# Performance work log

Measured on AMD Instinct MI355X. Metric: run time of the kernel, lower is better.

Reference implementation:

```python
import jax, jax.numpy as jnp
import numpy as np

B, IN, O = 256, 512, 10
STRUCTURES = list(range(32, 257, 32))  # 8 neuron structures
REPS, N_ACT = 4, 4


def _build_hidden_ids():
    ids = []
    i = 0
    # activation-major, then repetition, then structure (matches build_model_ids)
    for _ in range(N_ACT * REPS):
        for s in STRUCTURES:
            ids += [i] * s
            i += 1
    return np.asarray(ids, dtype=np.int32), i


def setup_inputs() -> dict:
    ids, M = _build_hidden_ids()
    H = len(ids)  # 18432
    k = jax.random.split(jax.random.key(0), 5)
    x = jax.random.normal(k[0], (B, IN), dtype=jnp.float32)
    hidden_w = jax.random.normal(k[1], (H, IN), dtype=jnp.float32) / np.sqrt(IN)
    hidden_b = jax.random.normal(k[2], (H,), dtype=jnp.float32) * 0.02
    out_w = jax.random.normal(k[3], (O, H), dtype=jnp.float32) * 0.05
    out_b = jax.random.normal(k[4], (M, O), dtype=jnp.float32) * 0.02
    return {"x": x, "hidden_w": hidden_w, "hidden_b": hidden_b,
            "out_w": out_w, "out_b": out_b,
            "hidden_ids": jnp.asarray(ids)}


_ACTS = [jax.nn.relu, jnp.tanh, jax.nn.sigmoid, lambda t: t]


def reference(x, hidden_w, hidden_b, out_w, out_b, hidden_ids):
    # hidden layer: [B, H]
    h = x @ hidden_w.T + hidden_b
    # per-activation contiguous splits (equal size H // n_act)
    chunks = jnp.split(h, N_ACT, axis=1)
    a = jnp.concatenate([f(c) for f, c in zip(_ACTS, chunks)], axis=1)  # [B, H]
    # per-hidden-neuron contribution to each output unit: [B, H, O]
    contrib = a[:, :, None] * out_w.T[None, :, :]
    M = out_b.shape[0]
    # segment-reduce hidden neurons into their model id: [M, B, O] -> [B, M, O]
    agg = jax.ops.segment_sum(contrib.transpose(1, 0, 2), hidden_ids, num_segments=M)
    return agg.transpose(1, 0, 2) + out_b[None, :, :]
```

## Files before the change

kernel.cpp:

```cpp
#include <hip/hip_runtime.h>
#include <hip/hip_bf16.h>

typedef __bf16 bf16x8 __attribute__((ext_vector_type(8)));
typedef float floatx4 __attribute__((ext_vector_type(4)));

#define BATCH 256
#define INDIM 512
#define ODIM 10
#define HTOT 18432
#define NMODEL 128
#define HTILE 64
#define BTILE 64
#define BK 64
#define LSTRIDE 72
#define ACT_CHUNK 4608
#define NJPG (HTOT / 32)

__device__ __forceinline__ unsigned pk2(float a, float b) {
    unsigned ua = __float_as_uint(a);
    ua = (ua + 0x7fffu + ((ua >> 16) & 1u)) >> 16;
    unsigned ub = __float_as_uint(b);
    ub = (ub + 0x7fffu + ((ub >> 16) & 1u)) >> 16;
    return ua | (ub << 16);
}

__device__ __forceinline__ float apply_act(float h, int aidx) {
    if (aidx == 0) return fmaxf(h, 0.f);
    if (aidx == 1) return 1.f - 2.f / (1.f + __expf(2.f * h));
    if (aidx == 2) return 1.f / (1.f + __expf(-h));
    return h;
}

__global__ __launch_bounds__(256, 4) void mlp_kernel(
    const float* __restrict__ x, const float* __restrict__ hidden_w,
    const float* __restrict__ hidden_b, const float* __restrict__ out_w,
    float* __restrict__ ws)
{
    __shared__ unsigned short xs[BTILE * LSTRIDE];
    __shared__ unsigned short wsx[HTILE * LSTRIDE];
    __shared__ float wtile[ODIM * HTILE];
    __shared__ float btile[HTILE];

    const int tid = threadIdx.x;
    const int bid = blockIdx.x;
    const int jb = bid >> 2, bb = bid & 3;
    const int j0 = jb * HTILE;
    const int b0 = bb * BTILE;
    const int lane = tid & 63;
    const int wvid = tid >> 6;
    const int r = lane & 15;
    const int g = lane >> 4;

    for (int i = tid; i < ODIM * HTILE; i += 256)
        wtile[i] = out_w[(i >> 6) * HTOT + j0 + (i & 63)];
    if (tid < HTILE) btile[tid] = hidden_b[j0 + tid];

    floatx4 acc[4];
    #pragma unroll
    for (int jt = 0; jt < 4; jt++) acc[jt] = (floatx4)0.f;

    const floatx4* xv  = (const floatx4*)x;
    const floatx4* wv4 = (const floatx4*)hidden_w;

    for (int kk = 0; kk < INDIM; kk += BK) {
        const int kq = kk >> 2;
        #pragma unroll
        for (int i = 0; i < 4; i++) {
            int f = tid + i * 256;
            int row = f >> 4, c4 = f & 15;
            floatx4 v = xv[(size_t)(b0 + row) * (INDIM / 4) + kq + c4];
            floatx4 u = wv4[(size_t)(j0 + row) * (INDIM / 4) + kq + c4];
            *(uint2*)&xs[row * LSTRIDE + c4 * 4]  = make_uint2(pk2(v[0], v[1]), pk2(v[2], v[3]));
            *(uint2*)&wsx[row * LSTRIDE + c4 * 4] = make_uint2(pk2(u[0], u[1]), pk2(u[2], u[3]));
        }
        __syncthreads();

        #pragma unroll
        for (int s = 0; s < 2; s++) {
            bf16x8 bfr = *(const bf16x8*)&xs[(wvid * 16 + r) * LSTRIDE + s * 32 + g * 8];
            #pragma unroll
            for (int jt = 0; jt < 4; jt++) {
                bf16x8 af = *(const bf16x8*)&wsx[(jt * 16 + r) * LSTRIDE + s * 32 + g * 8];
                acc[jt] = __builtin_amdgcn_mfma_f32_16x16x32_bf16(af, bfr, acc[jt], 0, 0, 0);
            }
        }
        __syncthreads();
    }

    const int aidx = j0 / ACT_CHUNK;
    const int b = b0 + wvid * 16 + r;

    #pragma unroll
    for (int jp = 0; jp < 2; jp++) {
        const int jpg = (j0 >> 5) + jp;
        float a[2][4];
        #pragma unroll
        for (int h = 0; h < 2; h++) {
            int jt = jp * 2 + h;
            #pragma unroll
            for (int q = 0; q < 4; q++)
                a[h][q] = apply_act(acc[jt][q] + btile[jt * 16 + g * 4 + q], aidx);
        }
        #pragma unroll
        for (int o = 0; o < ODIM; o++) {
            float p = 0.f;
            #pragma unroll
            for (int h = 0; h < 2; h++) {
                int jt = jp * 2 + h;
                const float* wr = &wtile[o * HTILE + jt * 16 + g * 4];
                p += a[h][0] * wr[0] + a[h][1] * wr[1] + a[h][2] * wr[2] + a[h][3] * wr[3];
            }
            p += __shfl_xor(p, 16, 64);
            p += __shfl_xor(p, 32, 64);
            if (lane < 16)
                ws[((size_t)jpg * ODIM + o) * BATCH + b] = p;
        }
    }
}

__global__ __launch_bounds__(256) void finalize_kernel(
    const float* __restrict__ ws, const float* __restrict__ out_b,
    float* __restrict__ out)
{
    const int mo = blockIdx.x;
    const int m = mo / ODIM, o = mo - m * ODIM;
    const int b = threadIdx.x;
    const int rep = m >> 3, idx = m & 7;
    const int jp0 = rep * 36 + (idx * (idx + 1)) / 2;
    const int cnt = idx + 1;

    float s = out_b[mo];
    for (int c = 0; c < cnt; c++)
        s += ws[((size_t)(jp0 + c) * ODIM + o) * BATCH + b];
    out[((size_t)b * NMODEL + m) * ODIM + o] = s;
}

extern "C" void kernel_launch(void* const* d_in, const int* in_sizes, int n_in,
                              void* d_out, int out_size, void* d_ws, size_t ws_size,
                              hipStream_t stream) {
    const float* x   = (const float*)d_in[0];
    const float* hw  = (const float*)d_in[1];
    const float* hb  = (const float*)d_in[2];
    const float* ow  = (const float*)d_in[3];
    const float* ob  = (const float*)d_in[4];
    float* out = (float*)d_out;
    float* ws  = (float*)d_ws;

    mlp_kernel<<<(HTOT / HTILE) * (BATCH / BTILE), 256, 0, stream>>>(x, hw, hb, ow, ws);
    finalize_kernel<<<NMODEL * ODIM, 256, 0, stream>>>(ws, ob, out);
}
```

Before: 114.6 us.

## Pre-convert weights to bf16 and stream tiles via global_load_lds

```diff
diff --git a/kernel.cpp b/kernel.cpp
--- a/kernel.cpp
+++ b/kernel.cpp
@@ -11,10 +11,15 @@
 #define NMODEL 128
 #define HTILE 64
 #define BTILE 64
-#define BK 64
-#define LSTRIDE 72
+#define BK 32
 #define ACT_CHUNK 4608
+#define WCNT (HTOT * INDIM)
+#define XCNT (BATCH * INDIM)
 #define NJPG (HTOT / 32)
+
+#define GLOAD_LDS(gp, lp) __builtin_amdgcn_global_load_lds( \
+    (const __attribute__((address_space(1))) unsigned int*)(const void*)(gp), \
+    (__attribute__((address_space(3))) unsigned int*)(lp), 16, 0, 0)
 
 __device__ __forceinline__ unsigned pk2(float a, float b) {
     unsigned ua = __float_as_uint(a);
@@ -31,13 +36,27 @@
     return h;
 }
 
-__global__ __launch_bounds__(256, 4) void mlp_kernel(
-    const float* __restrict__ x, const float* __restrict__ hidden_w,
+__global__ __launch_bounds__(256) void convert_kernel(
+    const float* __restrict__ hw, const float* __restrict__ x,
+    unsigned short* __restrict__ dst)
+{
+    size_t i = (size_t)(blockIdx.x * 256 + threadIdx.x) * 8;
+    const float* src = (i < (size_t)WCNT) ? hw + i : x + (i - WCNT);
+    floatx4 v0 = *(const floatx4*)src;
+    floatx4 v1 = *(const floatx4*)(src + 4);
+    uint4 o;
+    o.x = pk2(v0[0], v0[1]); o.y = pk2(v0[2], v0[3]);
+    o.z = pk2(v1[0], v1[1]); o.w = pk2(v1[2], v1[3]);
+    *(uint4*)(dst + i) = o;
+}
+
+__global__ __launch_bounds__(256, 5) void mlp_kernel(
+    const unsigned short* __restrict__ wbf, const unsigned short* __restrict__ xbf,
     const float* __restrict__ hidden_b, const float* __restrict__ out_w,
-    float* __restrict__ ws)
+    float* __restrict__ part)
 {
-    __shared__ unsigned short xs[BTILE * LSTRIDE];
-    __shared__ unsigned short wsx[HTILE * LSTRIDE];
+    __shared__ __align__(16) unsigned short xs[BTILE * BK];
+    __shared__ __align__(16) unsigned short wsx[HTILE * BK];
     __shared__ float wtile[ODIM * HTILE];
     __shared__ float btile[HTILE];
 
@@ -59,30 +78,22 @@
     #pragma unroll
     for (int jt = 0; jt < 4; jt++) acc[jt] = (floatx4)0.f;
 
-    const floatx4* xv  = (const floatx4*)x;
-    const floatx4* wv4 = (const floatx4*)hidden_w;
+    const int srow = wvid * 16 + (lane >> 2);
+    const int scol = (lane & 3) * 8;
+    const unsigned short* gw = wbf + (size_t)(j0 + srow) * INDIM + scol;
+    const unsigned short* gx = xbf + (size_t)(b0 + srow) * INDIM + scol;
+    unsigned short* lw = &wsx[wvid * 16 * BK];
+    unsigned short* lx = &xs[wvid * 16 * BK];
 
     for (int kk = 0; kk < INDIM; kk += BK) {
-        const int kq = kk >> 2;
+        GLOAD_LDS(gw + kk, lw);
+        GLOAD_LDS(gx + kk, lx);
+        __syncthreads();
+        bf16x8 bfr = *(const bf16x8*)&xs[(wvid * 16 + r) * BK + g * 8];
         #pragma unroll
-        for (int i = 0; i < 4; i++) {
-            int f = tid + i * 256;
-            int row = f >> 4, c4 = f & 15;
-            floatx4 v = xv[(size_t)(b0 + row) * (INDIM / 4) + kq + c4];
-            floatx4 u = wv4[(size_t)(j0 + row) * (INDIM / 4) + kq + c4];
-            *(uint2*)&xs[row * LSTRIDE + c4 * 4]  = make_uint2(pk2(v[0], v[1]), pk2(v[2], v[3]));
-            *(uint2*)&wsx[row * LSTRIDE + c4 * 4] = make_uint2(pk2(u[0], u[1]), pk2(u[2], u[3]));
-        }
-        __syncthreads();
-
-        #pragma unroll
-        for (int s = 0; s < 2; s++) {
-            bf16x8 bfr = *(const bf16x8*)&xs[(wvid * 16 + r) * LSTRIDE + s * 32 + g * 8];
-            #pragma unroll
-            for (int jt = 0; jt < 4; jt++) {
-                bf16x8 af = *(const bf16x8*)&wsx[(jt * 16 + r) * LSTRIDE + s * 32 + g * 8];
-                acc[jt] = __builtin_amdgcn_mfma_f32_16x16x32_bf16(af, bfr, acc[jt], 0, 0, 0);
-            }
+        for (int jt = 0; jt < 4; jt++) {
+            bf16x8 af = *(const bf16x8*)&wsx[(jt * 16 + r) * BK + g * 8];
+            acc[jt] = __builtin_amdgcn_mfma_f32_16x16x32_bf16(af, bfr, acc[jt], 0, 0, 0);
         }
         __syncthreads();
     }
@@ -113,13 +124,13 @@
             p += __shfl_xor(p, 16, 64);
             p += __shfl_xor(p, 32, 64);
             if (lane < 16)
-                ws[((size_t)jpg * ODIM + o) * BATCH + b] = p;
+                part[((size_t)jpg * ODIM + o) * BATCH + b] = p;
         }
     }
 }
 
 __global__ __launch_bounds__(256) void finalize_kernel(
-    const float* __restrict__ ws, const float* __restrict__ out_b,
+    const float* __restrict__ part, const float* __restrict__ out_b,
     float* __restrict__ out)
 {
     const int mo = blockIdx.x;
@@ -131,7 +142,7 @@
 
     float s = out_b[mo];
     for (int c = 0; c < cnt; c++)
-        s += ws[((size_t)(jp0 + c) * ODIM + o) * BATCH + b];
+        s += part[((size_t)(jp0 + c) * ODIM + o) * BATCH + b];
     out[((size_t)b * NMODEL + m) * ODIM + o] = s;
 }
 
@@ -144,8 +155,12 @@
     const float* ow  = (const float*)d_in[3];
     const float* ob  = (const float*)d_in[4];
     float* out = (float*)d_out;
-    float* ws  = (float*)d_ws;
 
-    mlp_kernel<<<(HTOT / HTILE) * (BATCH / BTILE), 256, 0, stream>>>(x, hw, hb, ow, ws);
-    finalize_kernel<<<NMODEL * ODIM, 256, 0, stream>>>(ws, ob, out);
+    unsigned short* wbf = (unsigned short*)d_ws;
+    unsigned short* xbf = wbf + WCNT;
+    float* part = (float*)d_ws + (WCNT + XCNT) / 2;
+
+    convert_kernel<<<(WCNT + XCNT) / 8 / 256, 256, 0, stream>>>(hw, x, wbf);
+    mlp_kernel<<<(HTOT / HTILE) * (BATCH / BTILE), 256, 0, stream>>>(wbf, xbf, hb, ow, part);
+    finalize_kernel<<<NMODEL * ODIM, 256, 0, stream>>>(part, ob, out);
 }
```

Result: no change. 115.9 us (+1.1%).
